# Kernel optimization log

Hardware: AMD Instinct MI355X
Metric: run time of the kernel (lower is better)

Reference implementation:

```python
import jax, jax.numpy as jnp
import numpy as np

EPS = 1e-5


def gcn_conv(x, W, b, src, dst):
    """PyG GCNConv: transform, add self-loops, symmetric norm, scatter-add, bias."""
    N = x.shape[0]
    h = x @ W  # [N, out]
    loop = jnp.arange(N)
    s = jnp.concatenate([src, loop])  # sources incl. self-loops
    d = jnp.concatenate([dst, loop])  # targets incl. self-loops
    deg = jax.ops.segment_sum(jnp.ones(s.shape[0], h.dtype), d, num_segments=N)
    dis = jnp.where(deg > 0, jax.lax.rsqrt(deg), 0.0)  # deg^-1/2
    norm = dis[s] * dis[d]  # [E+N]
    out = jax.ops.segment_sum(h[s] * norm[:, None], d, num_segments=N)
    return out + b


def batchnorm(x, gamma, beta):
    mu = x.mean(axis=0)
    var = x.var(axis=0)
    return (x - mu) * jax.lax.rsqrt(var + EPS) * gamma + beta


def setup_inputs() -> dict:
    key = jax.random.key(0)
    ks = jax.random.split(key, 6)
    N, E = 100000, 1600000
    IN, HID, OUT = 128, 256, 64
    x = jax.random.normal(ks[0], (N, IN), dtype=jnp.float32)
    edge_index = jax.random.randint(ks[1], (2, E), 0, N, dtype=jnp.int64)
    W1 = jax.random.normal(ks[2], (IN, HID), dtype=jnp.float32) / np.sqrt(IN)
    b1 = jnp.zeros((HID,), jnp.float32)
    gamma1 = jnp.ones((HID,), jnp.float32)
    beta1 = jnp.zeros((HID,), jnp.float32)
    W2 = jax.random.normal(ks[3], (HID, OUT), dtype=jnp.float32) / np.sqrt(HID)
    b2 = jnp.zeros((OUT,), jnp.float32)
    return {"x": x, "edge_index": edge_index, "W1": W1, "b1": b1,
            "gamma1": gamma1, "beta1": beta1, "W2": W2, "b2": b2}


def reference(x, edge_index, W1, b1, gamma1, beta1, W2, b2):
    src, dst = edge_index[0], edge_index[1]
    h = gcn_conv(x, W1, b1, src, dst)
    h = jax.nn.relu(batchnorm(h, gamma1, beta1))
    # dropout is identity at inference
    return gcn_conv(h, W2, b2, src, dst)
```

## Files before the change

### kernel.cpp

```cpp
#include <hip/hip_runtime.h>
#include <hip/hip_bf16.h>


#define IN_F  128
#define HID_F 256
#define OUT_F 64
#define BK_SHIFT 8
#define BK_SIZE  256
#define CHUNK    8192

typedef unsigned int uint;
typedef unsigned short ushort;
typedef short bf16x8 __attribute__((ext_vector_type(8)));
typedef float f32x4 __attribute__((ext_vector_type(4)));

__device__ __forceinline__ ushort f2bf(float f) {
    uint u = __float_as_uint(f);
    uint r = (u + 0x7fffu + ((u >> 16) & 1u)) >> 16;
    return (ushort)r;
}
__device__ __forceinline__ float bf_lo(uint u) { return __uint_as_float(u << 16); }
__device__ __forceinline__ float bf_hi(uint u) { return __uint_as_float(u & 0xffff0000u); }


__global__ void bucket_hist_kernel(const int* __restrict__ dst, int* __restrict__ bhist,
                                   int E, int NB) {
    __shared__ int h[512];
    for (int i = threadIdx.x; i < NB; i += 256) h[i] = 0;
    __syncthreads();
    int base = blockIdx.x * CHUNK;
    int end = min(base + CHUNK, E);
    for (int i = base + threadIdx.x; i < end; i += 256)
        atomicAdd(&h[dst[i] >> BK_SHIFT], 1);
    __syncthreads();
    for (int i = threadIdx.x; i < NB; i += 256)
        if (h[i]) atomicAdd(&bhist[i], h[i]);
}

__global__ void bucket_scan_kernel(const int* __restrict__ bhist, int* __restrict__ bbase,
                                   int* __restrict__ bcursor, int NB, int E) {
    __shared__ int sh[512];
    int t = threadIdx.x;
    int v = (t < NB) ? bhist[t] : 0;
    sh[t] = v;
    __syncthreads();
    for (int off = 1; off < 512; off <<= 1) {
        int u = (t >= off) ? sh[t - off] : 0;
        __syncthreads();
        sh[t] += u;
        __syncthreads();
    }
    if (t < NB) { int b = sh[t] - v; bbase[t] = b; bcursor[t] = b; }
    if (t == 0) bbase[NB] = E;
}

__global__ void bucket_scatter_kernel(const int* __restrict__ src, const int* __restrict__ dst,
                                      int* __restrict__ bcursor, uint* __restrict__ ebuf,
                                      int E, int NB) {
    __shared__ int h[512];
    __shared__ int cur[512];
    for (int i = threadIdx.x; i < NB; i += 256) h[i] = 0;
    __syncthreads();
    int base = blockIdx.x * CHUNK;
    int end = min(base + CHUNK, E);
    for (int i = base + threadIdx.x; i < end; i += 256)
        atomicAdd(&h[dst[i] >> BK_SHIFT], 1);
    __syncthreads();
    for (int i = threadIdx.x; i < NB; i += 256)
        cur[i] = h[i] ? atomicAdd(&bcursor[i], h[i]) : 0;
    __syncthreads();
    for (int i = base + threadIdx.x; i < end; i += 256) {
        int d = dst[i], s = src[i];
        int b = d >> BK_SHIFT;
        int pos = atomicAdd(&cur[b], 1);
        ebuf[pos] = (uint)s | ((uint)(d & (BK_SIZE - 1)) << 24);
    }
}

__global__ void bucket_build_kernel(const uint* __restrict__ ebuf, const int* __restrict__ bbase,
                                    int* __restrict__ deg_e, int* __restrict__ offsets,
                                    float* __restrict__ dis, int* __restrict__ ssrc, int N) {
    __shared__ int cnt[256], off[256], cur[256];
    int b = blockIdx.x;
    int t = threadIdx.x;
    cnt[t] = 0;
    __syncthreads();
    int e0 = bbase[b], e1 = bbase[b + 1];
    for (int i = e0 + t; i < e1; i += 256)
        atomicAdd(&cnt[ebuf[i] >> 24], 1);
    __syncthreads();
    int v = cnt[t];
    int vpad = (v + 3) & ~3;
    off[t] = vpad;
    __syncthreads();
    for (int o = 1; o < 256; o <<= 1) {
        int u = (t >= o) ? off[t - o] : 0;
        __syncthreads();
        off[t] += u;
        __syncthreads();
    }
    int excl = off[t] - vpad;
    int base_pad = e0 + b * 768;
    int d = b * BK_SIZE + t;
    if (d < N) {
        deg_e[d] = vpad;
        offsets[d] = base_pad + excl;
        dis[d] = rsqrtf((float)(v + 1));
    }
    cur[t] = excl;
    __syncthreads();
    for (int i = e0 + t; i < e1; i += 256) {
        uint e = ebuf[i];
        int ld = e >> 24;
        int pos = atomicAdd(&cur[ld], 1);
        ssrc[base_pad + pos] = (int)(e & 0xFFFFFFu);
    }
    __syncthreads();
    for (int i = v; i < vpad; i++)
        ssrc[base_pad + excl + i] = N;
}

__global__ void prep_kernel(const float* __restrict__ x, const float* __restrict__ dis,
                            uint* __restrict__ xs, const float* __restrict__ W1,
                            const float* __restrict__ W2, ushort* __restrict__ W1bp,
                            ushort* __restrict__ W2bp, int N) {
    int b = blockIdx.x;
    if (b < 192) {
        int i = b * 256 + threadIdx.x;
        if (i < 32768) {
            int kk = i & 31, c = (i >> 5) & 255, kc = i >> 13;
            W1bp[i] = f2bf(W1[(size_t)(kc * 32 + kk) * HID_F + c]);
        } else {
            int j = i - 32768;
            int kk = j & 31, c = (j >> 5) & 63, kc = j >> 11;
            W2bp[j] = f2bf(W2[(size_t)(kc * 32 + kk) * OUT_F + c]);
        }
        return;
    }
    int i = (b - 192) * 256 + threadIdx.x;
    if (i < (N + 1) * (IN_F / 2)) {
        int n = i >> 6;
        if (n >= N) { xs[i] = 0u; return; }
        float dn = dis[n];
        float2 v = ((const float2*)x)[i];
        xs[i] = (uint)f2bf(dn * v.x) | ((uint)f2bf(dn * v.y) << 16);
    }
}


__global__ void aggx_kernel(const uint* __restrict__ xs, const int* __restrict__ ssrc,
                            const int* __restrict__ offsets, const int* __restrict__ deg_e,
                            const float* __restrict__ dis, uint* __restrict__ zb, int N) {
    int lane = threadIdx.x & 63;
    int n = blockIdx.x * 4 + (threadIdx.x >> 6);
    if (n >= N) return;
    int grp = lane >> 4;
    int ck = lane & 15;
    float acc[8];
#pragma unroll
    for (int i = 0; i < 8; i++) acc[i] = 0.f;
    int start = offsets[n], cnt = deg_e[n];
    for (int base = 0; base < cnt; base += 64) {
        int m = min(64, cnt - base);
        int idx = base + lane;
        int sv = ssrc[start + (idx < cnt ? idx : cnt - 1)];
        int rounds = m >> 2;
#pragma unroll 2
        for (int q = 0; q < rounds; q++) {
            int s = __shfl(sv, (q << 2) | grp);
            uint4 u = *(const uint4*)(xs + ((size_t)s << 6) + (ck << 2));
            acc[0] += bf_lo(u.x); acc[1] += bf_hi(u.x);
            acc[2] += bf_lo(u.y); acc[3] += bf_hi(u.y);
            acc[4] += bf_lo(u.z); acc[5] += bf_hi(u.z);
            acc[6] += bf_lo(u.w); acc[7] += bf_hi(u.w);
        }
    }
#pragma unroll
    for (int i = 0; i < 8; i++) acc[i] += __shfl_down(acc[i], 32);
#pragma unroll
    for (int i = 0; i < 8; i++) acc[i] += __shfl_down(acc[i], 16);
    if (grp == 0) {
        uint4 u = *(const uint4*)(xs + ((size_t)n << 6) + (ck << 2));
        acc[0] += bf_lo(u.x); acc[1] += bf_hi(u.x);
        acc[2] += bf_lo(u.y); acc[3] += bf_hi(u.y);
        acc[4] += bf_lo(u.z); acc[5] += bf_hi(u.z);
        acc[6] += bf_lo(u.w); acc[7] += bf_hi(u.w);
        float dn = dis[n];
        uint4 o;
        o.x = (uint)f2bf(dn * acc[0]) | ((uint)f2bf(dn * acc[1]) << 16);
        o.y = (uint)f2bf(dn * acc[2]) | ((uint)f2bf(dn * acc[3]) << 16);
        o.z = (uint)f2bf(dn * acc[4]) | ((uint)f2bf(dn * acc[5]) << 16);
        o.w = (uint)f2bf(dn * acc[6]) | ((uint)f2bf(dn * acc[7]) << 16);
        *(uint4*)(zb + ((size_t)n << 6) + (ck << 2)) = o;
    }
}

__global__ __launch_bounds__(256) void gemm1_kernel(const uint* __restrict__ zb,
                                                    const uint* __restrict__ W1bp,
                                                    const float* __restrict__ b1,
                                                    ushort* __restrict__ out1b,
                                                    float* __restrict__ bnsum, int N) {
    __shared__ uint A[64][68];
    int t = threadIdx.x;
    int n0 = blockIdx.x * 64;
    for (int i = t; i < 64 * 16; i += 256) {
        int r = i >> 4, q = i & 15;
        int node = n0 + r;
        uint4 v = make_uint4(0u, 0u, 0u, 0u);
        if (node < N) v = *(const uint4*)(zb + (size_t)node * 64 + q * 4);
        *(uint4*)(&A[r][q * 4]) = v;
    }
    __syncthreads();
    int wave = t >> 6, lane = t & 63;
    int quad = lane >> 4, lrow = lane & 15;
    f32x4 acc[4][4];
#pragma unroll
    for (int m = 0; m < 4; m++)
#pragma unroll
        for (int nt = 0; nt < 4; nt++) acc[m][nt] = (f32x4)(0.f);
#pragma unroll
    for (int kc = 0; kc < 4; kc++) {
        bf16x8 bfr[4];
#pragma unroll
        for (int nt = 0; nt < 4; nt++) {
            int c = wave * 64 + nt * 16 + lrow;
            bfr[nt] = *(const bf16x8*)(W1bp + ((size_t)(kc * 256 + c) * 16 + quad * 4));
        }
        bf16x8 afr[4];
#pragma unroll
        for (int m = 0; m < 4; m++)
            afr[m] = *(const bf16x8*)(&A[m * 16 + lrow][kc * 16 + quad * 4]);
#pragma unroll
        for (int m = 0; m < 4; m++)
#pragma unroll
            for (int nt = 0; nt < 4; nt++)
                acc[m][nt] = __builtin_amdgcn_mfma_f32_16x16x32_bf16(
                    afr[m], bfr[nt], acc[m][nt], 0, 0, 0);
    }
#pragma unroll
    for (int nt = 0; nt < 4; nt++) {
        int c = wave * 64 + nt * 16 + lrow;
        float bb = b1[c];
        float s = 0.f, q = 0.f;
#pragma unroll
        for (int m = 0; m < 4; m++) {
#pragma unroll
            for (int r = 0; r < 4; r++) {
                int node = n0 + m * 16 + quad * 4 + r;
                if (node < N) {
                    float v = acc[m][nt][r] + bb;
                    out1b[(size_t)node * HID_F + c] = f2bf(v);
                    s += v;
                    q = fmaf(v, v, q);
                }
            }
        }
        s += __shfl_down(s, 32); q += __shfl_down(q, 32);
        s += __shfl_down(s, 16); q += __shfl_down(q, 16);
        if (quad == 0) {
            atomicAdd(&bnsum[c], s);
            atomicAdd(&bnsum[256 + c], q);
        }
    }
}

__global__ __launch_bounds__(256) void gemm2_kernel(const ushort* __restrict__ out1b,
                                                    const uint* __restrict__ W2bp,
                                                    const float* __restrict__ dis,
                                                    const float* __restrict__ bnsums,
                                                    const float* __restrict__ gamma,
                                                    const float* __restrict__ beta,
                                                    ushort* __restrict__ gs, int N) {
    __shared__ uint A[64][132];
    __shared__ float bns[256], bnb[256];
    const uint* out1u = (const uint*)out1b;
    int t = threadIdx.x;
    int n0 = blockIdx.x * 64;
    if (blockIdx.x == 0 && t < 32) ((uint*)gs)[(size_t)N * 32 + t] = 0u;
    {
        float invN = 1.0f / (float)N;
        float mean = bnsums[t] * invN;
        float var = bnsums[256 + t] * invN - mean * mean;
        float sc = gamma[t] * rsqrtf(fmaxf(var, 0.f) + 1e-5f);
        bns[t] = sc;
        bnb[t] = beta[t] - mean * sc;
    }
    __syncthreads();
    for (int i = t; i < 64 * 64; i += 256) {
        int r = i >> 6, u2 = i & 63;
        int node = n0 + r;
        uint2 p = make_uint2(0u, 0u);
        if (node < N) {
            uint2 v = *(const uint2*)(out1u + (size_t)node * 128 + u2 * 2);
            float r0 = fmaxf(fmaf(bf_lo(v.x), bns[u2 * 4 + 0], bnb[u2 * 4 + 0]), 0.f);
            float r1 = fmaxf(fmaf(bf_hi(v.x), bns[u2 * 4 + 1], bnb[u2 * 4 + 1]), 0.f);
            float r2 = fmaxf(fmaf(bf_lo(v.y), bns[u2 * 4 + 2], bnb[u2 * 4 + 2]), 0.f);
            float r3 = fmaxf(fmaf(bf_hi(v.y), bns[u2 * 4 + 3], bnb[u2 * 4 + 3]), 0.f);
            p.x = (uint)f2bf(r0) | ((uint)f2bf(r1) << 16);
            p.y = (uint)f2bf(r2) | ((uint)f2bf(r3) << 16);
        }
        *(uint2*)(&A[r][u2 * 2]) = p;
    }
    __syncthreads();
    int wave = t >> 6, lane = t & 63;
    int quad = lane >> 4, lrow = lane & 15;
    int c = wave * 16 + lrow;
    f32x4 acc[4];
#pragma unroll
    for (int m = 0; m < 4; m++) acc[m] = (f32x4)(0.f);
#pragma unroll
    for (int kc = 0; kc < 8; kc++) {
        bf16x8 bfr = *(const bf16x8*)(W2bp + ((size_t)(kc * 64 + c) * 16 + quad * 4));
#pragma unroll
        for (int m = 0; m < 4; m++) {
            bf16x8 afr = *(const bf16x8*)(&A[m * 16 + lrow][kc * 16 + quad * 4]);
            acc[m] = __builtin_amdgcn_mfma_f32_16x16x32_bf16(afr, bfr, acc[m], 0, 0, 0);
        }
    }
#pragma unroll
    for (int m = 0; m < 4; m++) {
#pragma unroll
        for (int r = 0; r < 4; r++) {
            int node = n0 + m * 16 + quad * 4 + r;
            if (node < N) gs[(size_t)node * OUT_F + c] = f2bf(dis[node] * acc[m][r]);
        }
    }
}

__global__ void agg2_kernel(const uint* __restrict__ gs, const int* __restrict__ ssrc,
                            const int* __restrict__ offsets, const int* __restrict__ deg_e,
                            const float* __restrict__ dis, const float* __restrict__ b2,
                            float* __restrict__ out, int N) {
    int lane = threadIdx.x & 63;
    int n = blockIdx.x * 4 + (threadIdx.x >> 6);
    if (n >= N) return;
    int grp = lane >> 3;
    int ck = lane & 7;
    float acc[8];
#pragma unroll
    for (int i = 0; i < 8; i++) acc[i] = 0.f;
    int start = offsets[n], cnt = deg_e[n];
    for (int base = 0; base < cnt; base += 64) {
        int m = min(64, cnt - base);
        int idx = base + lane;
        int sv = ssrc[start + (idx < cnt ? idx : cnt - 1)];
        int rounds = m >> 3;
#pragma unroll 2
        for (int q = 0; q < rounds; q++) {
            int s = __shfl(sv, (q << 3) | grp);
            uint4 u = *(const uint4*)(gs + ((size_t)s << 5) + (ck << 2));
            acc[0] += bf_lo(u.x); acc[1] += bf_hi(u.x);
            acc[2] += bf_lo(u.y); acc[3] += bf_hi(u.y);
            acc[4] += bf_lo(u.z); acc[5] += bf_hi(u.z);
            acc[6] += bf_lo(u.w); acc[7] += bf_hi(u.w);
        }
        if (m & 4) {
            int s = __shfl(sv, (rounds << 3) | (grp & 3));
            s = (grp & 4) ? N : s;
            uint4 u = *(const uint4*)(gs + ((size_t)s << 5) + (ck << 2));
            acc[0] += bf_lo(u.x); acc[1] += bf_hi(u.x);
            acc[2] += bf_lo(u.y); acc[3] += bf_hi(u.y);
            acc[4] += bf_lo(u.z); acc[5] += bf_hi(u.z);
            acc[6] += bf_lo(u.w); acc[7] += bf_hi(u.w);
        }
    }
#pragma unroll
    for (int i = 0; i < 8; i++) acc[i] += __shfl_down(acc[i], 32);
#pragma unroll
    for (int i = 0; i < 8; i++) acc[i] += __shfl_down(acc[i], 16);
#pragma unroll
    for (int i = 0; i < 8; i++) acc[i] += __shfl_down(acc[i], 8);
    if (grp == 0) {
        uint4 u = *(const uint4*)(gs + ((size_t)n << 5) + (ck << 2));
        acc[0] += bf_lo(u.x); acc[1] += bf_hi(u.x);
        acc[2] += bf_lo(u.y); acc[3] += bf_hi(u.y);
        acc[4] += bf_lo(u.z); acc[5] += bf_hi(u.z);
        acc[6] += bf_lo(u.w); acc[7] += bf_hi(u.w);
        float dn = dis[n];
        float4 bb0 = *(const float4*)(b2 + ck * 8);
        float4 bb1 = *(const float4*)(b2 + ck * 8 + 4);
        float* op = out + (size_t)n * OUT_F + ck * 8;
        *(float4*)op = make_float4(fmaf(dn, acc[0], bb0.x), fmaf(dn, acc[1], bb0.y),
                                   fmaf(dn, acc[2], bb0.z), fmaf(dn, acc[3], bb0.w));
        *(float4*)(op + 4) = make_float4(fmaf(dn, acc[4], bb1.x), fmaf(dn, acc[5], bb1.y),
                                         fmaf(dn, acc[6], bb1.z), fmaf(dn, acc[7], bb1.w));
    }
}

extern "C" void kernel_launch(void* const* d_in, const int* in_sizes, int n_in,
                              void* d_out, int out_size, void* d_ws, size_t ws_size,
                              hipStream_t stream) {
    const float* x      = (const float*)d_in[0];
    const int*   edges  = (const int*)d_in[1];
    const float* W1     = (const float*)d_in[2];
    const float* b1     = (const float*)d_in[3];
    const float* gamma1 = (const float*)d_in[4];
    const float* beta1  = (const float*)d_in[5];
    const float* W2     = (const float*)d_in[6];
    const float* b2     = (const float*)d_in[7];
    float* out = (float*)d_out;

    int N = in_sizes[0] / IN_F;
    int E = in_sizes[1] / 2;
    const int* src = edges;
    const int* dst = edges + E;
    int NB = (N + BK_SIZE - 1) / BK_SIZE;
    int nchunks = (E + CHUNK - 1) / CHUNK;

    char* ws = (char*)d_ws;
    size_t off = 0;
    auto alloc = [&](size_t bytes) -> void* {
        void* p = ws + off;
        off += (bytes + 255) & ~(size_t)255;
        return p;
    };
    int*    deg_e   = (int*)alloc((size_t)N * 4);
    int*    offsets = (int*)alloc((size_t)N * 4);
    float*  dis     = (float*)alloc((size_t)(N + 1) * 4);
    int*    bhist   = (int*)alloc(512 * 4);
    int*    bbase   = (int*)alloc(513 * 4);
    int*    bcursor = (int*)alloc(512 * 4);
    int*    ssrc    = (int*)alloc(((size_t)E + 768 * 512 + 64) * 4);
    uint*   ebuf    = (uint*)alloc((size_t)E * 4);
    uint*   xs      = (uint*)alloc((size_t)(N + 1) * (IN_F / 2) * 4);
    uint*   zb      = (uint*)alloc((size_t)N * (IN_F / 2) * 4);
    ushort* out1b   = (ushort*)alloc((size_t)N * HID_F * 2);
    float*  bn      = (float*)alloc(2 * 256 * 4);
    ushort* W1bp    = (ushort*)alloc(4 * 256 * 32 * 2);
    ushort* W2bp    = (ushort*)alloc(8 * 64 * 32 * 2);
    ushort* gs      = (ushort*)zb;

    hipMemsetAsync(bhist, 0, 512 * 4, stream);
    hipMemsetAsync(bn, 0, 2 * 256 * 4, stream);

    bucket_hist_kernel<<<nchunks, 256, 0, stream>>>(dst, bhist, E, NB);
    bucket_scan_kernel<<<1, 512, 0, stream>>>(bhist, bbase, bcursor, NB, E);
    bucket_scatter_kernel<<<nchunks, 256, 0, stream>>>(src, dst, bcursor, ebuf, E, NB);
    bucket_build_kernel<<<NB, 256, 0, stream>>>(ebuf, bbase, deg_e, offsets, dis, ssrc, N);

    int xblocks = ((N + 1) * (IN_F / 2) + 255) / 256;
    prep_kernel<<<192 + xblocks, 256, 0, stream>>>(x, dis, xs, W1, W2, W1bp, W2bp, N);
    aggx_kernel<<<(N + 3) / 4, 256, 0, stream>>>(xs, ssrc, offsets, deg_e, dis, zb, N);
    gemm1_kernel<<<(N + 63) / 64, 256, 0, stream>>>(zb, (const uint*)W1bp, b1, out1b, bn, N);
    gemm2_kernel<<<(N + 63) / 64, 256, 0, stream>>>(out1b, (const uint*)W2bp, dis, bn,
                                                    gamma1, beta1, gs, N);
    agg2_kernel<<<(N + 3) / 4, 256, 0, stream>>>((const uint*)gs, ssrc, offsets, deg_e, dis,
                                                 b2, out, N);
}
```

Baseline: 380.2 us.

## Stage GEMM outputs through XOR-swizzled LDS and replace BN atomics with two-pass reduction

Both GEMM kernels now use XOR-swizzled shared-memory tiles for the A operand, aiming to avoid LDS bank conflicts without padding. Their outputs are packed into shared memory and written with coalesced 16-byte stores instead of scattered 2-byte stores. Per-block batchnorm partial sums go to a buffer and are reduced by two small kernels, which removes global float atomics and the memset but adds two launches. gemm2 also loads its input with 16-byte vector loads.

```diff
diff --git a/kernel.cpp b/kernel.cpp
--- a/kernel.cpp
+++ b/kernel.cpp
@@ -199,8 +199,8 @@
                                                     const uint* __restrict__ W1bp,
                                                     const float* __restrict__ b1,
                                                     ushort* __restrict__ out1b,
-                                                    float* __restrict__ bnsum, int N) {
-    __shared__ uint A[64][68];
+                                                    float* __restrict__ bnp, int N) {
+    __shared__ uint sbuf[8192];
     int t = threadIdx.x;
     int n0 = blockIdx.x * 64;
     for (int i = t; i < 64 * 16; i += 256) {
@@ -208,7 +208,8 @@
         int node = n0 + r;
         uint4 v = make_uint4(0u, 0u, 0u, 0u);
         if (node < N) v = *(const uint4*)(zb + (size_t)node * 64 + q * 4);
-        *(uint4*)(&A[r][q * 4]) = v;
+        int p = q ^ (r & 15);
+        *(uint4*)(&sbuf[r * 64 + p * 4]) = v;
     }
     __syncthreads();
     int wave = t >> 6, lane = t & 63;
@@ -228,8 +229,10 @@
         }
         bf16x8 afr[4];
 #pragma unroll
-        for (int m = 0; m < 4; m++)
-            afr[m] = *(const bf16x8*)(&A[m * 16 + lrow][kc * 16 + quad * 4]);
+        for (int m = 0; m < 4; m++) {
+            int p = (kc * 4 + quad) ^ lrow;
+            afr[m] = *(const bf16x8*)(&sbuf[(m * 16 + lrow) * 64 + p * 4]);
+        }
 #pragma unroll
         for (int m = 0; m < 4; m++)
 #pragma unroll
@@ -237,6 +240,7 @@
                 acc[m][nt] = __builtin_amdgcn_mfma_f32_16x16x32_bf16(
                     afr[m], bfr[nt], acc[m][nt], 0, 0, 0);
     }
+    __syncthreads();
 #pragma unroll
     for (int nt = 0; nt < 4; nt++) {
         int c = wave * 64 + nt * 16 + lrow;
@@ -246,60 +250,96 @@
         for (int m = 0; m < 4; m++) {
 #pragma unroll
             for (int r = 0; r < 4; r++) {
-                int node = n0 + m * 16 + quad * 4 + r;
-                if (node < N) {
-                    float v = acc[m][nt][r] + bb;
-                    out1b[(size_t)node * HID_F + c] = f2bf(v);
-                    s += v;
-                    q = fmaf(v, v, q);
-                }
+                int row = m * 16 + quad * 4 + r;
+                float v = acc[m][nt][r] + bb;
+                if (n0 + row < N) { s += v; q = fmaf(v, v, q); }
+                uint hv = (uint)f2bf(v);
+                uint pv = __shfl_xor(hv, 1);
+                if ((lrow & 1) == 0)
+                    sbuf[row * 128 + (c >> 1)] = hv | (pv << 16);
             }
         }
         s += __shfl_down(s, 32); q += __shfl_down(q, 32);
         s += __shfl_down(s, 16); q += __shfl_down(q, 16);
         if (quad == 0) {
-            atomicAdd(&bnsum[c], s);
-            atomicAdd(&bnsum[256 + c], q);
-        }
-    }
+            bnp[(size_t)blockIdx.x * 512 + c] = s;
+            bnp[(size_t)blockIdx.x * 512 + 256 + c] = q;
+        }
+    }
+    __syncthreads();
+    uint* out1g = (uint*)out1b;
+    for (int i = t; i < 2048; i += 256) {
+        int row = i >> 5;
+        if (n0 + row < N)
+            *(uint4*)(out1g + (size_t)(n0 + row) * 128 + (i & 31) * 4) =
+                *(const uint4*)(&sbuf[i * 4]);
+    }
+}
+
+__global__ void bnred1_kernel(const float* __restrict__ bnp, float* __restrict__ bnp2,
+                              int nblk) {
+    int g = blockIdx.x, t = threadIdx.x;
+    float s = 0.f, q = 0.f;
+    for (int b = g; b < nblk; b += 32) {
+        s += bnp[(size_t)b * 512 + t];
+        q += bnp[(size_t)b * 512 + 256 + t];
+    }
+    bnp2[g * 512 + t] = s;
+    bnp2[g * 512 + 256 + t] = q;
+}
+
+__global__ void bnred2_kernel(const float* __restrict__ bnp2, const float* __restrict__ gamma,
+                              const float* __restrict__ beta, float* __restrict__ bnsb, int N) {
+    int t = threadIdx.x;
+    float s = 0.f, q = 0.f;
+    for (int g = 0; g < 32; g++) {
+        s += bnp2[g * 512 + t];
+        q += bnp2[g * 512 + 256 + t];
+    }
+    float invN = 1.0f / (float)N;
+    float mean = s * invN;
+    float var = q * invN - mean * mean;
+    float sc = gamma[t] * rsqrtf(fmaxf(var, 0.f) + 1e-5f);
+    bnsb[t] = sc;
+    bnsb[256 + t] = beta[t] - mean * sc;
 }
 
 __global__ __launch_bounds__(256) void gemm2_kernel(const ushort* __restrict__ out1b,
                                                     const uint* __restrict__ W2bp,
                                                     const float* __restrict__ dis,
-                                                    const float* __restrict__ bnsums,
-                                                    const float* __restrict__ gamma,
-                                                    const float* __restrict__ beta,
+                                                    const float* __restrict__ bnsb,
                                                     ushort* __restrict__ gs, int N) {
-    __shared__ uint A[64][132];
+    __shared__ uint sbuf[8192];
     __shared__ float bns[256], bnb[256];
     const uint* out1u = (const uint*)out1b;
     int t = threadIdx.x;
     int n0 = blockIdx.x * 64;
     if (blockIdx.x == 0 && t < 32) ((uint*)gs)[(size_t)N * 32 + t] = 0u;
-    {
-        float invN = 1.0f / (float)N;
-        float mean = bnsums[t] * invN;
-        float var = bnsums[256 + t] * invN - mean * mean;
-        float sc = gamma[t] * rsqrtf(fmaxf(var, 0.f) + 1e-5f);
-        bns[t] = sc;
-        bnb[t] = beta[t] - mean * sc;
-    }
-    __syncthreads();
-    for (int i = t; i < 64 * 64; i += 256) {
-        int r = i >> 6, u2 = i & 63;
+    bns[t] = bnsb[t];
+    bnb[t] = bnsb[256 + t];
+    __syncthreads();
+    for (int i = t; i < 64 * 32; i += 256) {
+        int r = i >> 5, q = i & 31;
         int node = n0 + r;
-        uint2 p = make_uint2(0u, 0u);
+        uint4 v = make_uint4(0u, 0u, 0u, 0u);
         if (node < N) {
-            uint2 v = *(const uint2*)(out1u + (size_t)node * 128 + u2 * 2);
-            float r0 = fmaxf(fmaf(bf_lo(v.x), bns[u2 * 4 + 0], bnb[u2 * 4 + 0]), 0.f);
-            float r1 = fmaxf(fmaf(bf_hi(v.x), bns[u2 * 4 + 1], bnb[u2 * 4 + 1]), 0.f);
-            float r2 = fmaxf(fmaf(bf_lo(v.y), bns[u2 * 4 + 2], bnb[u2 * 4 + 2]), 0.f);
-            float r3 = fmaxf(fmaf(bf_hi(v.y), bns[u2 * 4 + 3], bnb[u2 * 4 + 3]), 0.f);
-            p.x = (uint)f2bf(r0) | ((uint)f2bf(r1) << 16);
-            p.y = (uint)f2bf(r2) | ((uint)f2bf(r3) << 16);
-        }
-        *(uint2*)(&A[r][u2 * 2]) = p;
+            uint4 w = *(const uint4*)(out1u + (size_t)node * 128 + q * 4);
+            int c0 = q * 8;
+            float r0 = fmaxf(fmaf(bf_lo(w.x), bns[c0 + 0], bnb[c0 + 0]), 0.f);
+            float r1 = fmaxf(fmaf(bf_hi(w.x), bns[c0 + 1], bnb[c0 + 1]), 0.f);
+            float r2 = fmaxf(fmaf(bf_lo(w.y), bns[c0 + 2], bnb[c0 + 2]), 0.f);
+            float r3 = fmaxf(fmaf(bf_hi(w.y), bns[c0 + 3], bnb[c0 + 3]), 0.f);
+            float r4 = fmaxf(fmaf(bf_lo(w.z), bns[c0 + 4], bnb[c0 + 4]), 0.f);
+            float r5 = fmaxf(fmaf(bf_hi(w.z), bns[c0 + 5], bnb[c0 + 5]), 0.f);
+            float r6 = fmaxf(fmaf(bf_lo(w.w), bns[c0 + 6], bnb[c0 + 6]), 0.f);
+            float r7 = fmaxf(fmaf(bf_hi(w.w), bns[c0 + 7], bnb[c0 + 7]), 0.f);
+            v.x = (uint)f2bf(r0) | ((uint)f2bf(r1) << 16);
+            v.y = (uint)f2bf(r2) | ((uint)f2bf(r3) << 16);
+            v.z = (uint)f2bf(r4) | ((uint)f2bf(r5) << 16);
+            v.w = (uint)f2bf(r6) | ((uint)f2bf(r7) << 16);
+        }
+        int p = (q & 16) | ((q & 15) ^ (r & 15));
+        *(uint4*)(&sbuf[r * 128 + p * 4]) = v;
     }
     __syncthreads();
     int wave = t >> 6, lane = t & 63;
@@ -313,17 +353,33 @@
         bf16x8 bfr = *(const bf16x8*)(W2bp + ((size_t)(kc * 64 + c) * 16 + quad * 4));
 #pragma unroll
         for (int m = 0; m < 4; m++) {
-            bf16x8 afr = *(const bf16x8*)(&A[m * 16 + lrow][kc * 16 + quad * 4]);
+            int q = kc * 4 + quad;
+            int p = (q & 16) | ((q & 15) ^ lrow);
+            bf16x8 afr = *(const bf16x8*)(&sbuf[(m * 16 + lrow) * 128 + p * 4]);
             acc[m] = __builtin_amdgcn_mfma_f32_16x16x32_bf16(afr, bfr, acc[m], 0, 0, 0);
         }
     }
+    __syncthreads();
 #pragma unroll
     for (int m = 0; m < 4; m++) {
 #pragma unroll
         for (int r = 0; r < 4; r++) {
-            int node = n0 + m * 16 + quad * 4 + r;
-            if (node < N) gs[(size_t)node * OUT_F + c] = f2bf(dis[node] * acc[m][r]);
-        }
+            int row = m * 16 + quad * 4 + r;
+            int node = n0 + row;
+            float dn = (node < N) ? dis[node] : 0.f;
+            uint hv = (uint)f2bf(dn * acc[m][r]);
+            uint pv = __shfl_xor(hv, 1);
+            if ((lrow & 1) == 0)
+                sbuf[row * 32 + (c >> 1)] = hv | (pv << 16);
+        }
+    }
+    __syncthreads();
+    uint* gsg = (uint*)gs;
+    for (int i = t; i < 512; i += 256) {
+        int row = i >> 3;
+        if (n0 + row < N)
+            *(uint4*)(gsg + (size_t)(n0 + row) * 32 + (i & 7) * 4) =
+                *(const uint4*)(&sbuf[i * 4]);
     }
 }
 
@@ -406,6 +462,7 @@
     const int* dst = edges + E;
     int NB = (N + BK_SIZE - 1) / BK_SIZE;
     int nchunks = (E + CHUNK - 1) / CHUNK;
+    int nblk1 = (N + 63) / 64;
 
     char* ws = (char*)d_ws;
     size_t off = 0;
@@ -425,13 +482,14 @@
     uint*   xs      = (uint*)alloc((size_t)(N + 1) * (IN_F / 2) * 4);
     uint*   zb      = (uint*)alloc((size_t)N * (IN_F / 2) * 4);
     ushort* out1b   = (ushort*)alloc((size_t)N * HID_F * 2);
-    float*  bn      = (float*)alloc(2 * 256 * 4);
+    float*  bnp     = (float*)alloc((size_t)nblk1 * 512 * 4);
+    float*  bnp2    = (float*)alloc(32 * 512 * 4);
+    float*  bnsb    = (float*)alloc(512 * 4);
     ushort* W1bp    = (ushort*)alloc(4 * 256 * 32 * 2);
     ushort* W2bp    = (ushort*)alloc(8 * 64 * 32 * 2);
     ushort* gs      = (ushort*)zb;
 
     hipMemsetAsync(bhist, 0, 512 * 4, stream);
-    hipMemsetAsync(bn, 0, 2 * 256 * 4, stream);
 
     bucket_hist_kernel<<<nchunks, 256, 0, stream>>>(dst, bhist, E, NB);
     bucket_scan_kernel<<<1, 512, 0, stream>>>(bhist, bbase, bcursor, NB, E);
@@ -441,9 +499,10 @@
     int xblocks = ((N + 1) * (IN_F / 2) + 255) / 256;
     prep_kernel<<<192 + xblocks, 256, 0, stream>>>(x, dis, xs, W1, W2, W1bp, W2bp, N);
     aggx_kernel<<<(N + 3) / 4, 256, 0, stream>>>(xs, ssrc, offsets, deg_e, dis, zb, N);
-    gemm1_kernel<<<(N + 63) / 64, 256, 0, stream>>>(zb, (const uint*)W1bp, b1, out1b, bn, N);
-    gemm2_kernel<<<(N + 63) / 64, 256, 0, stream>>>(out1b, (const uint*)W2bp, dis, bn,
-                                                    gamma1, beta1, gs, N);
+    gemm1_kernel<<<nblk1, 256, 0, stream>>>(zb, (const uint*)W1bp, b1, out1b, bnp, N);
+    bnred1_kernel<<<32, 256, 0, stream>>>(bnp, bnp2, nblk1);
+    bnred2_kernel<<<1, 256, 0, stream>>>(bnp2, gamma1, beta1, bnsb, N);
+    gemm2_kernel<<<nblk1, 256, 0, stream>>>(out1b, (const uint*)W2bp, dis, bnsb, gs, N);
     agg2_kernel<<<(N + 3) / 4, 256, 0, stream>>>((const uint*)gs, ssrc, offsets, deg_e, dis,
                                                  b2, out, N);
 }
```

After: 360.0 us. 5.3% less time.
